# Kernel optimization log

Measured on AMD Instinct MI355X. Metric: run time of the kernel, lower is better.

Reference implementation:

```python
import jax, jax.numpy as jnp
import numpy as np

N_RAYS = 32768
N_SAMPLES = N_RAYS * 32  # 1,048,576
FDIM = 32
HID = 64
RGB_HID = 64
THRESHOLD = 1e-4  # early_termination_threshold


def setup_inputs() -> dict:
    key = jax.random.key(0)
    ks = jax.random.split(key, 12)
    # ragged per-ray sample counts (avg 32), adjusted so total is exactly N_SAMPLES
    rng = np.random.default_rng(0)
    counts = rng.integers(8, 57, size=N_RAYS)
    delta = int(N_SAMPLES - counts.sum())
    if delta >= 0:
        counts[:delta] += 1
    else:
        counts[:(-delta)] -= 1
    starts = np.concatenate([[0], np.cumsum(counts)[:-1]])
    packing_info = jnp.asarray(np.stack([starts, counts], axis=1), dtype=jnp.int32)
    ray_ids = jnp.asarray(np.repeat(np.arange(N_RAYS), counts), dtype=jnp.int32)

    pos = jax.random.uniform(ks[0], (N_SAMPLES, 3), minval=-1.0, maxval=1.0)
    dirs = jax.random.normal(ks[1], (N_SAMPLES, 3))
    dirs = dirs / jnp.linalg.norm(dirs, axis=1, keepdims=True)
    dt = jax.random.uniform(ks[2], (N_SAMPLES, 1), minval=0.0, maxval=0.01)
    packed_samples = jnp.concatenate([pos, dirs, dt], axis=1)

    def lin(k, fi, fo):
        return jax.random.normal(k, (fi, fo)) / np.sqrt(fi)

    return {
        "packed_samples": packed_samples,
        "packing_info": packing_info,
        "ray_ids": ray_ids,
        "w1": lin(ks[3], 3, HID), "b1": jnp.zeros(HID),
        "w2": lin(ks[4], HID, FDIM), "b2": jnp.zeros(FDIM),
        "w_sigma": lin(ks[5], FDIM, 1), "b_sigma": jnp.zeros(1),
        "w_rgb1": lin(ks[6], FDIM + 3, RGB_HID), "b_rgb1": jnp.zeros(RGB_HID),
        "w_rgb2": lin(ks[7], RGB_HID, 3), "b_rgb2": jnp.zeros(3),
        "bg_color": jnp.ones(3),
    }


def reference(packed_samples, packing_info, ray_ids, w1, b1, w2, b2,
              w_sigma, b_sigma, w_rgb1, b_rgb1, w_rgb2, b_rgb2, bg_color):
    pos = packed_samples[:, :3]
    dirs = packed_samples[:, 3:6]
    dt = packed_samples[:, 6]

    # feature_module
    feats = jax.nn.relu(pos @ w1 + b1) @ w2 + b2            # [N, FDIM]
    # sigma_decoder
    sigma = jax.nn.softplus(feats @ w_sigma + b_sigma)[:, 0]  # [N]

    # NerfWeights: per-ray transmittance T_i = exp(-sum_{j<i in ray} sigma_j*dt_j),
    # weight_i = T_i * (1 - exp(-sigma_i*dt_i)), zeroed once T drops below threshold.
    tau = sigma * dt
    c_excl = jnp.cumsum(tau) - tau                           # exclusive global cumsum
    seg_base = c_excl[packing_info[:, 0]]                    # cumsum before each ray's start
    T = jnp.exp(-(c_excl - seg_base[ray_ids]))
    alpha = 1.0 - jnp.exp(-tau)
    weights = jnp.where(T > THRESHOLD, T * alpha, 0.0)       # [N]

    # rgb_decoder (masked gather in torch is a perf trick; weight==0 kills masked rgbs)
    h = jax.nn.relu(jnp.concatenate([feats, dirs], axis=1) @ w_rgb1 + b_rgb1)
    rgbs = jax.nn.sigmoid(h @ w_rgb2 + b_rgb2)               # [N, 3]

    contrib = rgbs * weights[:, None]
    rendered = jax.ops.segment_sum(contrib, ray_ids, num_segments=N_RAYS)   # [n_rays,3]
    opac = jax.ops.segment_sum(weights, ray_ids, num_segments=N_RAYS)       # [n_rays]
    return rendered + bg_color * (1.0 - opac[:, None])
```

## Files before the change

### kernel.cpp

```cpp
#include <hip/hip_runtime.h>
#include <hip/hip_bf16.h>
#include <math.h>
#include <stdint.h>

#define N_RAYS    32768
#define N_SAMPLES (N_RAYS * 32)
#define THRESH 0.0001f

typedef __attribute__((ext_vector_type(8))) __bf16 bf16x8;
typedef __attribute__((ext_vector_type(4))) float  f32x4;
typedef float f4a __attribute__((ext_vector_type(4), aligned(4)));

union FragU { __hip_bfloat162 h2[4]; uint32_t w[4]; bf16x8 v; };

__device__ inline __hip_bfloat162 pk2(float lo, float hi) {
    float2 t; t.x = lo; t.y = hi;
    return __float22bfloat162_rn(t);
}

__device__ inline bf16x8 pack8(const float* vals) {
    FragU u;
    u.h2[0] = pk2(vals[0], vals[1]);
    u.h2[1] = pk2(vals[2], vals[3]);
    u.h2[2] = pk2(vals[4], vals[5]);
    u.h2[3] = pk2(vals[6], vals[7]);
    return u.v;
}

__device__ inline float rcp_fast(float x) {
    float r;
    asm("v_rcp_f32 %0, %1" : "=v"(r) : "v"(x));
    return r;
}
__device__ inline float sigmoid_fast(float x) { return rcp_fast(1.0f + __expf(-x)); }
__device__ inline float softplus_fast(float x) {
    const float e = __expf(-fabsf(x));
    return fmaxf(x, 0.0f) + __logf(1.0f + e);
}

__global__ __launch_bounds__(256, 2) void nerf_mlp_mfma(
    const float* __restrict__ samples,
    const float* __restrict__ w1,
    const float* __restrict__ b1,
    const float* __restrict__ w2,
    const float* __restrict__ b2,
    const float* __restrict__ w_sigma,
    const float* __restrict__ b_sigma,
    const float* __restrict__ w_rgb1,
    const float* __restrict__ b_rgb1,
    const float* __restrict__ w_rgb2,
    const float* __restrict__ b_rgb2,
    float4* __restrict__ out)
{
    const int lane = threadIdx.x & 63;
    const int g    = lane >> 4;
    const int sl   = lane & 15;
    const int wgid = (blockIdx.x * blockDim.x + threadIdx.x) >> 6;
    const int base0 = wgid * 128;

    f4a sa[4][2], sb[4][2];
    {
        const float* sp0 = samples + (size_t)(base0 + sl) * 7;
        const float* sp1 = samples + (size_t)(base0 + 16 + sl) * 7;
        sa[0][0] = *(const f4a*)sp0;  sb[0][0] = *(const f4a*)(sp0 + 3);
        sa[0][1] = *(const f4a*)sp1;  sb[0][1] = *(const f4a*)(sp1 + 3);
    }

    bf16x8 A1[4], A2[2][2], Ar1a[4], Ar1b[4], Ar2[2], Ar2f;

    #pragma unroll
    for (int t = 0; t < 4; ++t) {
        float v[8] = {0,0,0,0,0,0,0,0};
        if (g == 0) {
            const int j = t*16 + sl;
            v[0] = w1[j]; v[1] = w1[64+j]; v[2] = w1[128+j]; v[3] = b1[j];
        }
        A1[t] = pack8(v);
    }
    #pragma unroll
    for (int t = 0; t < 2; ++t)
        #pragma unroll
        for (int c = 0; c < 2; ++c) {
            float v[8];
            #pragma unroll
            for (int q = 0; q < 8; ++q) {
                const int j = 16*(2*c + (q>>2)) + 4*g + (q&3);
                v[q] = w2[j*32 + t*16 + sl];
            }
            A2[t][c] = pack8(v);
        }
    #pragma unroll
    for (int t = 0; t < 4; ++t) {
        float v[8];
        #pragma unroll
        for (int q = 0; q < 8; ++q) {
            const int f = 16*(q>>2) + 4*g + (q&3);
            v[q] = w_rgb1[f*64 + t*16 + sl];
        }
        Ar1a[t] = pack8(v);
    }
    #pragma unroll
    for (int t = 0; t < 4; ++t) {
        float v[8] = {0,0,0,0,0,0,0,0};
        if (g == 0) {
            const int j = t*16 + sl;
            v[0] = w_rgb1[32*64 + j]; v[1] = w_rgb1[33*64 + j];
            v[2] = w_rgb1[34*64 + j]; v[3] = b_rgb1[j];
        }
        Ar1b[t] = pack8(v);
    }
    #pragma unroll
    for (int c = 0; c < 2; ++c) {
        float v[8];
        #pragma unroll
        for (int q = 0; q < 8; ++q) {
            const int hh = 16*(2*c + (q>>2)) + 4*g + (q&3);
            v[q] = (sl < 3) ? w_rgb2[hh*3 + sl] : 0.0f;
        }
        Ar2[c] = pack8(v);
    }
    {
        float v[8];
        #pragma unroll
        for (int q = 0; q < 8; ++q) {
            const int f = 16*(q>>2) + 4*g + (q&3);
            v[q] = (sl == 3) ? w_sigma[f] : 0.0f;
        }
        Ar2f = pack8(v);
    }
    f32x4 b2i[2];
    #pragma unroll
    for (int t = 0; t < 2; ++t)
        #pragma unroll
        for (int r = 0; r < 4; ++r)
            b2i[t][r] = b2[16*t + 4*g + r];
    f32x4 arinit;
    arinit[0] = b_rgb2[0]; arinit[1] = b_rgb2[1];
    arinit[2] = b_rgb2[2]; arinit[3] = b_sigma[0];

    const float biasone = (g == 0) ? 1.0f : 0.0f;
    const f32x4 zero4 = {0.f, 0.f, 0.f, 0.f};

    #pragma unroll
    for (int it = 0; it < 4; ++it) {
        if (it < 3) {
            const int nb = base0 + (it + 1) * 32;
            const float* sp0 = samples + (size_t)(nb + sl) * 7;
            const float* sp1 = samples + (size_t)(nb + 16 + sl) * 7;
            sa[it+1][0] = *(const f4a*)sp0;  sb[it+1][0] = *(const f4a*)(sp0 + 3);
            sa[it+1][1] = *(const f4a*)sp1;  sb[it+1][1] = *(const f4a*)(sp1 + 3);
        }

        FragU b1u[2], bd[2];
        #pragma unroll
        for (int s = 0; s < 2; ++s) {
            b1u[s].h2[0] = pk2(sa[it][s].x, sa[it][s].y);
            b1u[s].h2[1] = pk2(sa[it][s].z, biasone);
            b1u[s].w[2] = 0; b1u[s].w[3] = 0;
            bd[s].h2[0]  = pk2(sb[it][s].x, sb[it][s].y);
            bd[s].h2[1]  = pk2(sb[it][s].z, biasone);
            bd[s].w[2] = 0; bd[s].w[3] = 0;
        }

        f32x4 accL1[2][4];
        #pragma unroll
        for (int t = 0; t < 4; ++t)
            #pragma unroll
            for (int s = 0; s < 2; ++s)
                accL1[s][t] = __builtin_amdgcn_mfma_f32_16x16x32_bf16(A1[t], b1u[s].v, zero4, 0,0,0);

        FragU B2c[2][2];
        #pragma unroll
        for (int s = 0; s < 2; ++s)
            #pragma unroll
            for (int c = 0; c < 2; ++c) {
                B2c[s][c].h2[0] = pk2(fmaxf(accL1[s][2*c  ][0],0.f), fmaxf(accL1[s][2*c  ][1],0.f));
                B2c[s][c].h2[1] = pk2(fmaxf(accL1[s][2*c  ][2],0.f), fmaxf(accL1[s][2*c  ][3],0.f));
                B2c[s][c].h2[2] = pk2(fmaxf(accL1[s][2*c+1][0],0.f), fmaxf(accL1[s][2*c+1][1],0.f));
                B2c[s][c].h2[3] = pk2(fmaxf(accL1[s][2*c+1][2],0.f), fmaxf(accL1[s][2*c+1][3],0.f));
            }

        f32x4 accL2[2][2];
        #pragma unroll
        for (int t = 0; t < 2; ++t)
            #pragma unroll
            for (int s = 0; s < 2; ++s) {
                accL2[s][t] = __builtin_amdgcn_mfma_f32_16x16x32_bf16(A2[t][0], B2c[s][0].v, b2i[t], 0,0,0);
                accL2[s][t] = __builtin_amdgcn_mfma_f32_16x16x32_bf16(A2[t][1], B2c[s][1].v, accL2[s][t], 0,0,0);
            }
        FragU Bf[2];
        #pragma unroll
        for (int s = 0; s < 2; ++s) {
            Bf[s].h2[0] = pk2(accL2[s][0][0], accL2[s][0][1]);
            Bf[s].h2[1] = pk2(accL2[s][0][2], accL2[s][0][3]);
            Bf[s].h2[2] = pk2(accL2[s][1][0], accL2[s][1][1]);
            Bf[s].h2[3] = pk2(accL2[s][1][2], accL2[s][1][3]);
        }

        f32x4 ah[2][4];
        #pragma unroll
        for (int t = 0; t < 4; ++t)
            #pragma unroll
            for (int s = 0; s < 2; ++s) {
                ah[s][t] = __builtin_amdgcn_mfma_f32_16x16x32_bf16(Ar1a[t], Bf[s].v, zero4, 0,0,0);
                ah[s][t] = __builtin_amdgcn_mfma_f32_16x16x32_bf16(Ar1b[t], bd[s].v, ah[s][t], 0,0,0);
            }
        FragU Bh[2][2];
        #pragma unroll
        for (int s = 0; s < 2; ++s)
            #pragma unroll
            for (int c = 0; c < 2; ++c) {
                Bh[s][c].h2[0] = pk2(fmaxf(ah[s][2*c  ][0],0.f), fmaxf(ah[s][2*c  ][1],0.f));
                Bh[s][c].h2[1] = pk2(fmaxf(ah[s][2*c  ][2],0.f), fmaxf(ah[s][2*c  ][3],0.f));
                Bh[s][c].h2[2] = pk2(fmaxf(ah[s][2*c+1][0],0.f), fmaxf(ah[s][2*c+1][1],0.f));
                Bh[s][c].h2[3] = pk2(fmaxf(ah[s][2*c+1][2],0.f), fmaxf(ah[s][2*c+1][3],0.f));
            }

        f32x4 ar[2];
        #pragma unroll
        for (int s = 0; s < 2; ++s) {
            ar[s] = __builtin_amdgcn_mfma_f32_16x16x32_bf16(Ar2[0], Bh[s][0].v, arinit, 0,0,0);
            ar[s] = __builtin_amdgcn_mfma_f32_16x16x32_bf16(Ar2[1], Bh[s][1].v, ar[s], 0,0,0);
            ar[s] = __builtin_amdgcn_mfma_f32_16x16x32_bf16(Ar2f,   Bf[s].v,    ar[s], 0,0,0);
        }

        #pragma unroll
        for (int s = 0; s < 2; ++s) {
            const float rr    = sigmoid_fast(ar[s][0]);
            const float gg    = sigmoid_fast(ar[s][1]);
            const float bb    = sigmoid_fast(ar[s][2]);
            const float sigma = softplus_fast(ar[s][3]);
            const float tau   = sigma * sb[it][s].w;
            if (g == 0) out[base0 + it * 32 + s * 16 + sl] = make_float4(tau, rr, gg, bb);
        }
    }
}

__global__ __launch_bounds__(256) void nerf_render_kernel(
    const float4* __restrict__ smp,
    const int*    __restrict__ packing,
    const float*  __restrict__ bg,
    float*        __restrict__ out)
{
    const int gtid = blockIdx.x * blockDim.x + threadIdx.x;
    const int ray  = gtid >> 6;
    const int lane = threadIdx.x & 63;
    if (ray >= N_RAYS) return;

    const int start = packing[2 * ray];
    const int count = packing[2 * ray + 1];

    float tau = 0.0f, r = 0.0f, g = 0.0f, b = 0.0f;
    if (lane < count) {
        const float4 v = smp[start + lane];
        tau = v.x; r = v.y; g = v.z; b = v.w;
    }

    float incl = tau;
    #pragma unroll
    for (int off = 1; off < 64; off <<= 1) {
        const float v = __shfl_up(incl, off, 64);
        if (lane >= off) incl += v;
    }
    const float c_excl = incl - tau;

    const float T     = __expf(-c_excl);
    const float alpha = 1.0f - __expf(-tau);
    float w = (lane < count && T > THRESH) ? T * alpha : 0.0f;

    float cr = r * w, cg = g * w, cb = b * w;

    #pragma unroll
    for (int off = 32; off > 0; off >>= 1) {
        cr += __shfl_down(cr, off, 64);
        cg += __shfl_down(cg, off, 64);
        cb += __shfl_down(cb, off, 64);
        w  += __shfl_down(w,  off, 64);
    }

    if (lane == 0) {
        out[ray * 3 + 0] = cr + bg[0] * (1.0f - w);
        out[ray * 3 + 1] = cg + bg[1] * (1.0f - w);
        out[ray * 3 + 2] = cb + bg[2] * (1.0f - w);
    }
}

extern "C" void kernel_launch(void* const* d_in, const int* in_sizes, int n_in,
                              void* d_out, int out_size, void* d_ws, size_t ws_size,
                              hipStream_t stream) {
    const float* samples  = (const float*)d_in[0];
    const int*   packing  = (const int*)  d_in[1];
    const float* w1       = (const float*)d_in[3];
    const float* b1       = (const float*)d_in[4];
    const float* w2       = (const float*)d_in[5];
    const float* b2       = (const float*)d_in[6];
    const float* w_sigma  = (const float*)d_in[7];
    const float* b_sigma  = (const float*)d_in[8];
    const float* w_rgb1   = (const float*)d_in[9];
    const float* b_rgb1   = (const float*)d_in[10];
    const float* w_rgb2   = (const float*)d_in[11];
    const float* b_rgb2   = (const float*)d_in[12];
    const float* bg       = (const float*)d_in[13];

    float4* smp = (float4*)d_ws;
    float*  out = (float*)d_out;

    nerf_mlp_mfma<<<2048, 256, 0, stream>>>(
        samples, w1, b1, w2, b2, w_sigma, b_sigma,
        w_rgb1, b_rgb1, w_rgb2, b_rgb2, smp);

    nerf_render_kernel<<<(N_RAYS * 64) / 256, 256, 0, stream>>>(smp, packing, bg, out);
}
```

Before: 53.62 us.

## Prebuild packed bf16 weight fragments in a setup kernel and raise occupancy

Adds a tiny single-block kernel that packs all MLP weights and biases into per-lane bf16 MFMA fragments stored in workspace. The main MLP kernel now loads each fragment with one 16-byte coalesced load instead of many scattered scalar loads plus conversions in every wavefront, which frees registers. Launch bounds are raised to allow 4 blocks per CU. The cost is an extra kernel launch and a dependency on workspace being large enough at the 16MB offset.

```diff
diff --git a/kernel.cpp b/kernel.cpp
--- a/kernel.cpp
+++ b/kernel.cpp
@@ -6,12 +6,15 @@
 #define N_RAYS    32768
 #define N_SAMPLES (N_RAYS * 32)
 #define THRESH 0.0001f
+#define TBL_OFF  (16u * 1024u * 1024u)
+#define N_FRAGS  22
 
 typedef __attribute__((ext_vector_type(8))) __bf16 bf16x8;
 typedef __attribute__((ext_vector_type(4))) float  f32x4;
 typedef float f4a __attribute__((ext_vector_type(4), aligned(4)));
 
 union FragU { __hip_bfloat162 h2[4]; uint32_t w[4]; bf16x8 v; };
+union RecU  { bf16x8 v; f32x4 f; uint4 u; };
 
 __device__ inline __hip_bfloat162 pk2(float lo, float hi) {
     float2 t; t.x = lo; t.y = hi;
@@ -38,18 +41,100 @@
     return fmaxf(x, 0.0f) + __logf(1.0f + e);
 }
 
-__global__ __launch_bounds__(256, 2) void nerf_mlp_mfma(
+__global__ __launch_bounds__(256) void nerf_build_frags(
+    const float* __restrict__ w1,  const float* __restrict__ b1,
+    const float* __restrict__ w2,  const float* __restrict__ b2,
+    const float* __restrict__ w_sigma, const float* __restrict__ b_sigma,
+    const float* __restrict__ w_rgb1,  const float* __restrict__ b_rgb1,
+    const float* __restrict__ w_rgb2,  const float* __restrict__ b_rgb2,
+    uint4* __restrict__ tbl)
+{
+    const int wid  = threadIdx.x >> 6;
+    const int lane = threadIdx.x & 63;
+    const int g    = lane >> 4;
+    const int sl   = lane & 15;
+    RecU rec;
+
+    if (wid == 0) {
+        #pragma unroll
+        for (int t = 0; t < 4; ++t) {
+            float v[8] = {0,0,0,0,0,0,0,0};
+            if (g == 0) {
+                const int j = t*16 + sl;
+                v[0] = w1[j]; v[1] = w1[64+j]; v[2] = w1[128+j]; v[3] = b1[j];
+            }
+            rec.v = pack8(v); tbl[t*64 + lane] = rec.u;
+        }
+        #pragma unroll
+        for (int t = 0; t < 2; ++t)
+            #pragma unroll
+            for (int c = 0; c < 2; ++c) {
+                float v[8];
+                #pragma unroll
+                for (int q = 0; q < 8; ++q) {
+                    const int j = 16*(2*c + (q>>2)) + 4*g + (q&3);
+                    v[q] = w2[j*32 + t*16 + sl];
+                }
+                rec.v = pack8(v); tbl[(4 + 2*t + c)*64 + lane] = rec.u;
+            }
+    } else if (wid == 1) {
+        #pragma unroll
+        for (int t = 0; t < 4; ++t) {
+            float v[8];
+            #pragma unroll
+            for (int q = 0; q < 8; ++q) {
+                const int f = 16*(q>>2) + 4*g + (q&3);
+                v[q] = w_rgb1[f*64 + t*16 + sl];
+            }
+            rec.v = pack8(v); tbl[(8 + t)*64 + lane] = rec.u;
+        }
+        #pragma unroll
+        for (int t = 0; t < 4; ++t) {
+            float v[8] = {0,0,0,0,0,0,0,0};
+            if (g == 0) {
+                const int j = t*16 + sl;
+                v[0] = w_rgb1[32*64 + j]; v[1] = w_rgb1[33*64 + j];
+                v[2] = w_rgb1[34*64 + j]; v[3] = b_rgb1[j];
+            }
+            rec.v = pack8(v); tbl[(12 + t)*64 + lane] = rec.u;
+        }
+    } else if (wid == 2) {
+        #pragma unroll
+        for (int c = 0; c < 2; ++c) {
+            float v[8];
+            #pragma unroll
+            for (int q = 0; q < 8; ++q) {
+                const int hh = 16*(2*c + (q>>2)) + 4*g + (q&3);
+                v[q] = (sl < 3) ? w_rgb2[hh*3 + sl] : 0.0f;
+            }
+            rec.v = pack8(v); tbl[(16 + c)*64 + lane] = rec.u;
+        }
+        {
+            float v[8];
+            #pragma unroll
+            for (int q = 0; q < 8; ++q) {
+                const int f = 16*(q>>2) + 4*g + (q&3);
+                v[q] = (sl == 3) ? w_sigma[f] : 0.0f;
+            }
+            rec.v = pack8(v); tbl[18*64 + lane] = rec.u;
+        }
+        #pragma unroll
+        for (int t = 0; t < 2; ++t) {
+            #pragma unroll
+            for (int r = 0; r < 4; ++r) rec.f[r] = b2[16*t + 4*g + r];
+            tbl[(19 + t)*64 + lane] = rec.u;
+        }
+        {
+            rec.f[0] = b_rgb2[0]; rec.f[1] = b_rgb2[1];
+            rec.f[2] = b_rgb2[2]; rec.f[3] = b_sigma[0];
+            tbl[21*64 + lane] = rec.u;
+        }
+    }
+}
+
+__global__ __launch_bounds__(256, 4) void nerf_mlp_mfma(
     const float* __restrict__ samples,
-    const float* __restrict__ w1,
-    const float* __restrict__ b1,
-    const float* __restrict__ w2,
-    const float* __restrict__ b2,
-    const float* __restrict__ w_sigma,
-    const float* __restrict__ b_sigma,
-    const float* __restrict__ w_rgb1,
-    const float* __restrict__ b_rgb1,
-    const float* __restrict__ w_rgb2,
-    const float* __restrict__ b_rgb2,
+    const uint4* __restrict__ tbl,
     float4* __restrict__ out)
 {
     const int lane = threadIdx.x & 63;
@@ -67,76 +152,26 @@
     }
 
     bf16x8 A1[4], A2[2][2], Ar1a[4], Ar1b[4], Ar2[2], Ar2f;
-
-    #pragma unroll
-    for (int t = 0; t < 4; ++t) {
-        float v[8] = {0,0,0,0,0,0,0,0};
-        if (g == 0) {
-            const int j = t*16 + sl;
-            v[0] = w1[j]; v[1] = w1[64+j]; v[2] = w1[128+j]; v[3] = b1[j];
-        }
-        A1[t] = pack8(v);
-    }
-    #pragma unroll
-    for (int t = 0; t < 2; ++t)
-        #pragma unroll
-        for (int c = 0; c < 2; ++c) {
-            float v[8];
-            #pragma unroll
-            for (int q = 0; q < 8; ++q) {
-                const int j = 16*(2*c + (q>>2)) + 4*g + (q&3);
-                v[q] = w2[j*32 + t*16 + sl];
-            }
-            A2[t][c] = pack8(v);
-        }
-    #pragma unroll
-    for (int t = 0; t < 4; ++t) {
-        float v[8];
-        #pragma unroll
-        for (int q = 0; q < 8; ++q) {
-            const int f = 16*(q>>2) + 4*g + (q&3);
-            v[q] = w_rgb1[f*64 + t*16 + sl];
-        }
-        Ar1a[t] = pack8(v);
-    }
-    #pragma unroll
-    for (int t = 0; t < 4; ++t) {
-        float v[8] = {0,0,0,0,0,0,0,0};
-        if (g == 0) {
-            const int j = t*16 + sl;
-            v[0] = w_rgb1[32*64 + j]; v[1] = w_rgb1[33*64 + j];
-            v[2] = w_rgb1[34*64 + j]; v[3] = b_rgb1[j];
-        }
-        Ar1b[t] = pack8(v);
-    }
-    #pragma unroll
-    for (int c = 0; c < 2; ++c) {
-        float v[8];
-        #pragma unroll
-        for (int q = 0; q < 8; ++q) {
-            const int hh = 16*(2*c + (q>>2)) + 4*g + (q&3);
-            v[q] = (sl < 3) ? w_rgb2[hh*3 + sl] : 0.0f;
-        }
-        Ar2[c] = pack8(v);
-    }
+    f32x4 b2i[2], arinit;
     {
-        float v[8];
-        #pragma unroll
-        for (int q = 0; q < 8; ++q) {
-            const int f = 16*(q>>2) + 4*g + (q&3);
-            v[q] = (sl == 3) ? w_sigma[f] : 0.0f;
-        }
-        Ar2f = pack8(v);
-    }
-    f32x4 b2i[2];
-    #pragma unroll
-    for (int t = 0; t < 2; ++t)
-        #pragma unroll
-        for (int r = 0; r < 4; ++r)
-            b2i[t][r] = b2[16*t + 4*g + r];
-    f32x4 arinit;
-    arinit[0] = b_rgb2[0]; arinit[1] = b_rgb2[1];
-    arinit[2] = b_rgb2[2]; arinit[3] = b_sigma[0];
+        RecU r_;
+        #pragma unroll
+        for (int t = 0; t < 4; ++t) { r_.u = tbl[t*64 + lane];       A1[t]   = r_.v; }
+        #pragma unroll
+        for (int t = 0; t < 2; ++t)
+            #pragma unroll
+            for (int c = 0; c < 2; ++c) { r_.u = tbl[(4+2*t+c)*64 + lane]; A2[t][c] = r_.v; }
+        #pragma unroll
+        for (int t = 0; t < 4; ++t) { r_.u = tbl[(8+t)*64 + lane];   Ar1a[t] = r_.v; }
+        #pragma unroll
+        for (int t = 0; t < 4; ++t) { r_.u = tbl[(12+t)*64 + lane];  Ar1b[t] = r_.v; }
+        #pragma unroll
+        for (int c = 0; c < 2; ++c) { r_.u = tbl[(16+c)*64 + lane];  Ar2[c]  = r_.v; }
+        r_.u = tbl[18*64 + lane]; Ar2f = r_.v;
+        r_.u = tbl[19*64 + lane]; b2i[0] = r_.f;
+        r_.u = tbl[20*64 + lane]; b2i[1] = r_.f;
+        r_.u = tbl[21*64 + lane]; arinit = r_.f;
+    }
 
     const float biasone = (g == 0) ? 1.0f : 0.0f;
     const f32x4 zero4 = {0.f, 0.f, 0.f, 0.f};
@@ -303,11 +338,14 @@
     const float* bg       = (const float*)d_in[13];
 
     float4* smp = (float4*)d_ws;
+    uint4*  tbl = (uint4*)((char*)d_ws + TBL_OFF);
     float*  out = (float*)d_out;
 
-    nerf_mlp_mfma<<<2048, 256, 0, stream>>>(
-        samples, w1, b1, w2, b2, w_sigma, b_sigma,
-        w_rgb1, b_rgb1, w_rgb2, b_rgb2, smp);
+    nerf_build_frags<<<1, 256, 0, stream>>>(
+        w1, b1, w2, b2, w_sigma, b_sigma,
+        w_rgb1, b_rgb1, w_rgb2, b_rgb2, tbl);
+
+    nerf_mlp_mfma<<<2048, 256, 0, stream>>>(samples, tbl, (float4*)smp);
 
     nerf_render_kernel<<<(N_RAYS * 64) / 256, 256, 0, stream>>>(smp, packing, bg, out);
 }
```

Result: slower. 60.42 us (+12.7%).
